# Optimization experiments

Measured on AMD Instinct MI355X. Metric: run time of the kernel, lower is better.

Reference implementation:

```python
import jax, jax.numpy as jnp
import numpy as np

E, A, K = 8192, 128, 512  # parallel_envs, num_agents, passengers per env
P = E * K                 # total passengers (global table rows)


def setup_inputs() -> dict:
    key = jax.random.key(0)
    k1, k2, k3, k4, k5, k6 = jax.random.split(key, 6)
    passengers = jax.random.normal(k1, (P, 11), dtype=jnp.float32)
    # column 0 is the env index of each passenger (used to gather timesteps)
    passengers = passengers.at[:, 0].set(jnp.repeat(jnp.arange(E, dtype=jnp.float32), K))
    accepts = jax.random.bernoulli(k2, 0.5, (E, A))
    picks = jax.random.bernoulli(k3, 0.3, (E, A))
    # env-partitioned global passenger indices: row e targets in [e*K, (e+1)*K)
    local_t = jax.random.randint(k4, (E, A), 0, K, dtype=jnp.int32)
    targets = jnp.arange(E, dtype=jnp.int32)[:, None] * K + local_t
    vectors = jax.random.normal(k5, (E, A, 4), dtype=jnp.float32)
    # give a quarter of agents zero src->dst distance so the pick branch fires
    vectors = vectors.at[:, : A // 4, 2:4].set(vectors[:, : A // 4, 0:2])
    # mark last 8 agent slots per env as invalid (all -100)
    vectors = vectors.at[:, -8:, :].set(-100.0)
    timesteps = jax.random.randint(k6, (E,), 0, 1000, dtype=jnp.int32)
    return {"passengers": passengers, "accepts": accepts, "picks": picks,
            "targets": targets, "vectors": vectors, "timesteps": timesteps}


def _distances(vectors):
    d = jnp.sqrt(((vectors[:, :, 0:2] - vectors[:, :, 2:4]) ** 2).sum(-1))
    return jnp.where((vectors == -100.0).all(-1), jnp.inf, d)


def _dup_mask(t, P):
    # torch: unique(return_inverse, return_counts) -> counts[inverse] > 1 & t != -100
    seg = jnp.where(t >= 0, t, P).ravel()  # -100 -> sentinel bucket P
    counts = jax.ops.segment_sum(jnp.ones(seg.shape, jnp.int32), seg, num_segments=P + 1)
    return (counts[seg].reshape(t.shape) > 1) & (t >= 0)


def reference(passengers, accepts, picks, targets, vectors, timesteps):
    E_, A_ = targets.shape
    P_ = passengers.shape[0]

    distances = _distances(vectors)
    accept_t = jnp.where(accepts, targets, -100)

    def cond(carry):
        t, _ = carry
        return _dup_mask(t, P_).any()

    def body(carry):
        t, d = carry
        dup = _dup_mask(t, P_)
        d = jnp.where(dup, d, jnp.inf)  # cumulative, as in torch
        keep = jnp.arange(A_)[None, :] == jnp.argmin(d, axis=1)[:, None]
        t = jnp.where(dup & ~keep, -100, t)
        return t, d

    accept_t, _ = jax.lax.while_loop(cond, body, (accept_t, distances))

    # scatter accept results into passenger table (at most one agent per passenger now)
    valid = accept_t >= 0
    seg = jnp.where(valid, accept_t, P_).ravel()
    accepted = jax.ops.segment_sum(valid.astype(jnp.int32).ravel(), seg, num_segments=P_ + 1)[:P_] > 0
    agent_ids = jnp.broadcast_to(jnp.arange(A_, dtype=jnp.int32)[None, :], (E_, A_))
    agent_of = jax.ops.segment_max(jnp.where(valid, agent_ids, -100).ravel(), seg, num_segments=P_ + 1)[:P_]
    ts = timesteps[passengers[:, 0].astype(jnp.int32)].astype(passengers.dtype)  # per-passenger timestep

    p = passengers
    p = p.at[:, 6].set(jnp.where(accepted, 1.0, p[:, 6]))
    p = p.at[:, 9].set(jnp.where(accepted, ts, p[:, 9]))
    p = p.at[:, 7].set(jnp.where(accepted, agent_of.astype(p.dtype), p[:, 7]))

    # pick transition: only zero-distance picks succeed
    d2 = _distances(vectors)
    pick_t = jnp.where(picks, targets, -100)
    pd = jnp.where(pick_t >= 0, d2, jnp.inf)
    pick_t = jnp.where(pd < 1e-6, pick_t, -100)
    pvalid = pick_t >= 0
    pseg = jnp.where(pvalid, pick_t, P_).ravel()
    picked = jax.ops.segment_sum(pvalid.astype(jnp.int32).ravel(), pseg, num_segments=P_ + 1)[:P_] > 0
    p = p.at[:, 6].set(jnp.where(picked, 2.0, p[:, 6]))
    p = p.at[:, 10].set(jnp.where(picked, ts, p[:, 10]))
    return p
```

## Files before the change

### kernel.cpp

```cpp
#include <hip/hip_runtime.h>

#define E_ENV  8192
#define A_AG   128
#define K_PASS 512
#define ROW_F  11
#define SLICE_F  (K_PASS * ROW_F)
#define SLICE_V4 (SLICE_F / 4)
#define ITERS    (SLICE_V4 / A_AG)

__global__ __launch_bounds__(128) void k_fused(
    const float4* __restrict__ pass4,
    const int*    __restrict__ accepts,
    const int*    __restrict__ picks,
    const int*    __restrict__ targets,
    const float4* __restrict__ vectors,
    const int*    __restrict__ timesteps,
    float4*       __restrict__ out4)
{
    __shared__ int           cnt[K_PASS];
    __shared__ int           agentOf[K_PASS];
    __shared__ unsigned char pickF[K_PASS];
    __shared__ float swv[2];
    __shared__ int   swi[2];

    const int e   = blockIdx.x;
    const int a   = threadIdx.x;
    const int gid = e * A_AG + a;

    #pragma unroll
    for (int j = 0; j < K_PASS / A_AG; ++j) {
        cnt[a + j * A_AG]     = 0;
        agentOf[a + j * A_AG] = -1;
        pickF[a + j * A_AG]   = 0;
    }
    __syncthreads();

    float4 v = vectors[gid];
    bool invalid = (v.x == -100.0f) && (v.y == -100.0f) &&
                   (v.z == -100.0f) && (v.w == -100.0f);
    float dx = v.x - v.z, dy = v.y - v.w;
    float d = sqrtf(dx * dx + dy * dy);
    if (invalid) d = INFINITY;

    const int  t    = targets[gid];
    const int  tl   = t - e * K_PASS;
    const bool acc  = accepts[gid] != 0;
    const bool pick = picks[gid] != 0;

    int at = acc ? t : -100;
    if (at >= 0) atomicAdd(&cnt[tl], 1);
    __syncthreads();

    bool dup = (at >= 0) && (cnt[tl] > 1);
    float bv = dup ? d : INFINITY;
    int   bi = a;

    #pragma unroll
    for (int off = 32; off > 0; off >>= 1) {
        float ov = __shfl_xor(bv, off);
        int   oi = __shfl_xor(bi, off);
        if (ov < bv || (ov == bv && oi < bi)) { bv = ov; bi = oi; }
    }
    int wave = a >> 6;
    if ((a & 63) == 0) { swv[wave] = bv; swi[wave] = bi; }
    __syncthreads();
    float v0 = swv[0], v1 = swv[1];
    int   i0 = swi[0], i1 = swi[1];
    int bidx = (v1 < v0 || (v1 == v0 && i1 < i0)) ? i1 : i0;

    int f = (dup && a != bidx) ? -100 : at;

    if (f >= 0) agentOf[tl] = a;
    if (pick && d < 1e-6f) pickF[tl] = 1;
    __syncthreads();

    const float tsf = (float)timesteps[e];

    const float4* src = pass4 + (size_t)e * SLICE_V4;
    float4*       dst = out4  + (size_t)e * SLICE_V4;

    auto patch = [&](float val, unsigned row, int col) -> float {
        if (col == 6) {
            if (pickF[row]) return 2.0f;
            if (agentOf[row] >= 0) return 1.0f;
        } else if (col == 7) {
            int ag = agentOf[row];
            if (ag >= 0) return (float)ag;
        } else if (col == 9) {
            if (agentOf[row] >= 0) return tsf;
        } else if (col == 10) {
            if (pickF[row]) return tsf;
        }
        return val;
    };

    int idx = a;
    #pragma unroll
    for (int it = 0; it < ITERS; ++it, idx += A_AG) {
        float4 x = src[idx];
        unsigned g   = (unsigned)idx * 4u;
        unsigned row = g / 11u;
        int      col = (int)(g - row * 11u);
        x.x = patch(x.x, row, col); if (++col == 11) { col = 0; ++row; }
        x.y = patch(x.y, row, col); if (++col == 11) { col = 0; ++row; }
        x.z = patch(x.z, row, col); if (++col == 11) { col = 0; ++row; }
        x.w = patch(x.w, row, col);
        dst[idx] = x;
    }
}

extern "C" void kernel_launch(void* const* d_in, const int* in_sizes, int n_in,
                              void* d_out, int out_size, void* d_ws, size_t ws_size,
                              hipStream_t stream)
{
    const float* passengers = (const float*)d_in[0];
    const int*   accepts    = (const int*)d_in[1];
    const int*   picks      = (const int*)d_in[2];
    const int*   targets    = (const int*)d_in[3];
    const float* vectors    = (const float*)d_in[4];
    const int*   timesteps  = (const int*)d_in[5];
    float*       out        = (float*)d_out;

    k_fused<<<E_ENV, A_AG, 0, stream>>>(
        (const float4*)passengers, accepts, picks, targets,
        (const float4*)vectors, timesteps, (float4*)out);
}
```

Before: 346.8 us.

## Prefetch passenger slice into registers and scatter-patch only the changed rows

The kernel now issues all eleven float4 loads of the env's passenger slice into registers at the start, before the shared-memory setup and reductions, so global load latency overlaps that work. It writes the slice back unchanged, then after a barrier scatters scalar writes for columns 6, 7, 9 and 10 of accepted or picked passengers only. This drops the per-element division by 11, the column branching and the shared-memory lookups that ran in the copy loop. In exchange it uses more registers per thread and adds small scattered global stores. Correctness depends on the barrier ordering each block's copy stores before its patch stores to the same addresses.

```diff
diff --git a/kernel.cpp b/kernel.cpp
--- a/kernel.cpp
+++ b/kernel.cpp
@@ -15,7 +15,8 @@
     const int*    __restrict__ targets,
     const float4* __restrict__ vectors,
     const int*    __restrict__ timesteps,
-    float4*       __restrict__ out4)
+    float4*       __restrict__ out4,
+    float*        __restrict__ out)
 {
     __shared__ int           cnt[K_PASS];
     __shared__ int           agentOf[K_PASS];
@@ -27,6 +28,18 @@
     const int a   = threadIdx.x;
     const int gid = e * A_AG + a;
 
+    const float4* src = pass4 + (size_t)e * SLICE_V4;
+    float4*       dst = out4  + (size_t)e * SLICE_V4;
+    float4 x[ITERS];
+    #pragma unroll
+    for (int it = 0; it < ITERS; ++it)
+        x[it] = src[a + it * A_AG];
+
+    float4 v = vectors[gid];
+    const int  t    = targets[gid];
+    const bool acc  = accepts[gid] != 0;
+    const bool pick = picks[gid] != 0;
+
     #pragma unroll
     for (int j = 0; j < K_PASS / A_AG; ++j) {
         cnt[a + j * A_AG]     = 0;
@@ -35,17 +48,13 @@
     }
     __syncthreads();
 
-    float4 v = vectors[gid];
     bool invalid = (v.x == -100.0f) && (v.y == -100.0f) &&
                    (v.z == -100.0f) && (v.w == -100.0f);
     float dx = v.x - v.z, dy = v.y - v.w;
     float d = sqrtf(dx * dx + dy * dy);
     if (invalid) d = INFINITY;
 
-    const int  t    = targets[gid];
-    const int  tl   = t - e * K_PASS;
-    const bool acc  = accepts[gid] != 0;
-    const bool pick = picks[gid] != 0;
+    const int tl = t - e * K_PASS;
 
     int at = acc ? t : -100;
     if (at >= 0) atomicAdd(&cnt[tl], 1);
@@ -72,40 +81,28 @@
 
     if (f >= 0) agentOf[tl] = a;
     if (pick && d < 1e-6f) pickF[tl] = 1;
+
+    #pragma unroll
+    for (int it = 0; it < ITERS; ++it)
+        dst[a + it * A_AG] = x[it];
+
     __syncthreads();
 
     const float tsf = (float)timesteps[e];
-
-    const float4* src = pass4 + (size_t)e * SLICE_V4;
-    float4*       dst = out4  + (size_t)e * SLICE_V4;
-
-    auto patch = [&](float val, unsigned row, int col) -> float {
-        if (col == 6) {
-            if (pickF[row]) return 2.0f;
-            if (agentOf[row] >= 0) return 1.0f;
-        } else if (col == 7) {
-            int ag = agentOf[row];
-            if (ag >= 0) return (float)ag;
-        } else if (col == 9) {
-            if (agentOf[row] >= 0) return tsf;
-        } else if (col == 10) {
-            if (pickF[row]) return tsf;
+    #pragma unroll
+    for (int j = 0; j < K_PASS / A_AG; ++j) {
+        int p  = a + j * A_AG;
+        int ag = agentOf[p];
+        bool pk = pickF[p] != 0;
+        if (ag >= 0 || pk) {
+            size_t b = ((size_t)e * K_PASS + p) * ROW_F;
+            out[b + 6] = pk ? 2.0f : 1.0f;
+            if (ag >= 0) {
+                out[b + 7] = (float)ag;
+                out[b + 9] = tsf;
+            }
+            if (pk) out[b + 10] = tsf;
         }
-        return val;
-    };
-
-    int idx = a;
-    #pragma unroll
-    for (int it = 0; it < ITERS; ++it, idx += A_AG) {
-        float4 x = src[idx];
-        unsigned g   = (unsigned)idx * 4u;
-        unsigned row = g / 11u;
-        int      col = (int)(g - row * 11u);
-        x.x = patch(x.x, row, col); if (++col == 11) { col = 0; ++row; }
-        x.y = patch(x.y, row, col); if (++col == 11) { col = 0; ++row; }
-        x.z = patch(x.z, row, col); if (++col == 11) { col = 0; ++row; }
-        x.w = patch(x.w, row, col);
-        dst[idx] = x;
     }
 }
 
@@ -123,5 +120,5 @@
 
     k_fused<<<E_ENV, A_AG, 0, stream>>>(
         (const float4*)passengers, accepts, picks, targets,
-        (const float4*)vectors, timesteps, (float4*)out);
+        (const float4*)vectors, timesteps, (float4*)out, out);
 }
```

Result: slower. 380.7 us (+9.8%).
